# Kernel optimization log

Measured on AMD Instinct MI355X. Metric: run time of the kernel, lower is better.

Reference implementation:

```python
import jax, jax.numpy as jnp
import numpy as np

STEPS = 32
LO, HI = 0.0, 1.0
BETA = 0.1
IMPULSE = float(1.0 / (abs(BETA) * np.sqrt(np.pi)))  # unused in fwd, kept for parity


def _cells(x):
    """Filtration values of all cells of the V-construction cubical complex.
    Vertices = pixels; edges = max of the 2 endpoint pixels; squares = max of 4 corners."""
    v = x                                                    # [B,C,H,W]   sign +1
    he = jnp.maximum(x[..., :, :-1], x[..., :, 1:])          # [B,C,H,W-1] sign -1
    ve = jnp.maximum(x[..., :-1, :], x[..., 1:, :])          # [B,C,H-1,W] sign -1
    sq = jnp.maximum(jnp.maximum(x[..., :-1, :-1], x[..., :-1, 1:]),
                     jnp.maximum(x[..., 1:, :-1], x[..., 1:, 1:]))  # [B,C,H-1,W-1] sign +1
    return v, he, ve, sq


def _ecc_forward(x):
    """Euler characteristic curve ECC(t) = #V(t) - #E(t) + #F(t) sampled on
    tseq = linspace(LO, HI, STEPS). Returns [B, C*STEPS] (flattened, matching nn.Flatten)."""
    B, C, H, W = x.shape
    BC = B * C
    tseq = jnp.linspace(LO, HI, STEPS, dtype=x.dtype)
    v, he, ve, sq = _cells(x)
    f = jnp.concatenate([v.reshape(BC, -1), he.reshape(BC, -1),
                         ve.reshape(BC, -1), sq.reshape(BC, -1)], axis=1)  # [BC, Ncells]
    signs = jnp.concatenate([
        jnp.ones(H * W, jnp.float32),
        -jnp.ones(H * (W - 1), jnp.float32),
        -jnp.ones((H - 1) * W, jnp.float32),
        jnp.ones((H - 1) * (W - 1), jnp.float32),
    ])
    # first threshold index j with tseq[j] >= f (cell is "alive" for all t >= idx)
    idx = jnp.searchsorted(tseq, f, side='left')            # [BC, Ncells], values in [0, STEPS]
    rows = jnp.arange(BC)[:, None]
    hist = jnp.zeros((BC, STEPS + 1), jnp.float32).at[rows, idx].add(signs[None, :])
    ecc = jnp.cumsum(hist[:, :STEPS], axis=1)               # [BC, STEPS]
    return ecc.reshape(B, C * STEPS)


def setup_inputs() -> dict:
    key = jax.random.key(0)
    x = jax.random.uniform(key, (64, 3, 224, 224), dtype=jnp.float32)
    return {"x": x}


def reference(x):
    return _ecc_forward(x)
```

## Files before the change

### kernel.cpp

```cpp
#include <hip/hip_runtime.h>
#include <hip/hip_bf16.h>


#define H 224
#define W 224
#define STEPS 32
#define NBINS 33
#define NCOL 64
#define BANDS 8
#define BAND_ROWS 28
#define SUB_ROWS 7
#define NTHR 256

__device__ __forceinline__ int bin_of(float f) {
    return (int)fmaf(f, 31.0f, 0.99999994f);
}

struct BinState {
    int B0, B1, B2, B3, Bn, Bp;
};

__device__ __forceinline__ void pair1_update(int* __restrict__ lhc,
                                             const BinState& S)
{
    int dm = (S.B0 > S.Bp) ? 1 : 0;
    int d0 = (S.B1 > S.B0) ? 1 : 0;
    int d1 = (S.B2 > S.B1) ? 1 : 0;
    int d2 = (S.B3 > S.B2) ? 1 : 0;
    int d3 = (S.Bn > S.B3) ? 1 : 0;
    atomicAdd(&lhc[S.B0 << 6], d0 - dm);
    atomicAdd(&lhc[S.B1 << 6], d1 - d0);
    atomicAdd(&lhc[S.B2 << 6], d2 - d1);
    atomicAdd(&lhc[S.B3 << 6], d3 - d2);
}

__device__ __forceinline__ void pair2_update_roll(int* __restrict__ lhc,
                                                  BinState& S, float4 G,
                                                  bool lastc, bool firstc)
{
    int C0 = bin_of(G.x), C1 = bin_of(G.y), C2 = bin_of(G.z), C3 = bin_of(G.w);
    int t;
    t = __shfl_down(C0, 1); int Cn = lastc  ? 64 : t;
    t = __shfl_up  (C3, 1); int Cp = firstc ? 63 : t;

    int M0 = max(S.B0, C0), M1 = max(S.B1, C1),
        M2 = max(S.B2, C2), M3 = max(S.B3, C3);
    int Mn = max(S.Bn, Cn), Mp = max(S.Bp, Cp);
    int em = (M0 > Mp) ? 1 : 0;
    int e0 = (M1 > M0) ? 1 : 0;
    int e1 = (M2 > M1) ? 1 : 0;
    int e2 = (M3 > M2) ? 1 : 0;
    int e3 = (Mn > M3) ? 1 : 0;
    atomicAdd(&lhc[M0 << 6], em - e0);
    atomicAdd(&lhc[M1 << 6], e0 - e1);
    atomicAdd(&lhc[M2 << 6], e1 - e2);
    atomicAdd(&lhc[M3 << 6], e2 - e3);

    S.B0 = C0; S.B1 = C1; S.B2 = C2; S.B3 = C3; S.Bn = Cn; S.Bp = Cp;
}

__global__ __launch_bounds__(NTHR, 6) void ecc_fused_kernel(
        const float* __restrict__ x, float* __restrict__ out)
{
    __shared__ int lh[NBINS * NCOL];
    __shared__ int bins[STEPS];

    const int tid = threadIdx.x;
    for (int i = tid; i < NBINS * NCOL; i += NTHR) lh[i] = 0;
    __syncthreads();

    const int band = blockIdx.x & (BANDS - 1);
    const int img  = blockIdx.x / BANDS;
    const float* __restrict__ p = x + (size_t)img * (H * W);

    const int c = tid & 63;
    const int s = tid >> 6;

    if (c < 56) {
        const bool lastc  = (c == 55);
        const bool firstc = (c == 0);
        const int  r0 = band * BAND_ROWS + s * SUB_ROWS;
        int* __restrict__ lhc = lh + c;

        const float* __restrict__ row = p + r0 * W + (c << 2);
        float4 F = *(const float4*)row;
        BinState S;
        S.B0 = bin_of(F.x); S.B1 = bin_of(F.y);
        S.B2 = bin_of(F.z); S.B3 = bin_of(F.w);
        int t;
        t = __shfl_down(S.B0, 1); S.Bn = lastc  ? 64 : t;
        t = __shfl_up  (S.B3, 1); S.Bp = firstc ? 63 : t;

        if (r0 != H - SUB_ROWS) {
            #pragma unroll
            for (int k = 0; k < SUB_ROWS; ++k) {
                pair1_update(lhc, S);
                float4 G = *(const float4*)(row + W);
                pair2_update_roll(lhc, S, G, lastc, firstc);
                row += W;
            }
        } else {
            #pragma unroll
            for (int k = 0; k < SUB_ROWS - 1; ++k) {
                pair1_update(lhc, S);
                float4 G = *(const float4*)(row + W);
                pair2_update_roll(lhc, S, G, lastc, firstc);
                row += W;
            }
            pair1_update(lhc, S);
        }
    }
    __syncthreads();

    const int b = tid >> 3;
    const int g = tid & 7;
    const int4* rowp = (const int4*)(lh + (b << 6) + (g << 3));
    int4 u0 = rowp[0], u1 = rowp[1];
    int sum = u0.x + u0.y + u0.z + u0.w + u1.x + u1.y + u1.z + u1.w;
    sum += __shfl_xor(sum, 1);
    sum += __shfl_xor(sum, 2);
    sum += __shfl_xor(sum, 4);
    if (g == 0) bins[b] = sum;
    __syncthreads();

    if (tid < STEPS) {
        int v = bins[tid];
        #pragma unroll
        for (int off = 1; off < STEPS; off <<= 1) {
            int u = __shfl_up(v, off);
            if (tid >= off) v += u;
        }
        atomicAdd(&out[img * STEPS + tid], (float)v);
    }
}

extern "C" void kernel_launch(void* const* d_in, const int* in_sizes, int n_in,
                              void* d_out, int out_size, void* d_ws, size_t ws_size,
                              hipStream_t stream) {
    const float* x = (const float*)d_in[0];
    float* out = (float*)d_out;

    const int nimg = in_sizes[0] / (H * W);

    dim3 grid(nimg * BANDS);
    ecc_fused_kernel<<<grid, NTHR, 0, stream>>>(x, out);
}
```

Baseline: 75.44 us.

## Replace LDS atomics with private per-thread packed 16-bit histogram slabs

Each thread now owns a private column in a per-subrow slab, so histogram updates become plain read-modify-write instead of LDS atomicAdd. Two bins are packed per 32-bit word as biased 16-bit counters, which halves the number of words per slab. The final reduction unpacks and sums the four slabs and subtracts the bias. The cost is extra shift and mask work in the reduction and a reliance on the bias keeping each packed counter from underflowing or carrying into its neighbour.

```diff
diff --git a/kernel.cpp b/kernel.cpp
--- a/kernel.cpp
+++ b/kernel.cpp
@@ -1,26 +1,31 @@
 #include <hip/hip_runtime.h>
-#include <hip/hip_bf16.h>
 
 
 #define H 224
 #define W 224
 #define STEPS 32
-#define NBINS 33
+#define NWORDS 17
 #define NCOL 64
+#define SLAB (NWORDS * NCOL)
 #define BANDS 8
 #define BAND_ROWS 28
 #define SUB_ROWS 7
 #define NTHR 256
+#define BIASW 0x00400040
 
 __device__ __forceinline__ int bin_of(float f) {
     return (int)fmaf(f, 31.0f, 0.99999994f);
+}
+
+__device__ __forceinline__ void hist_add(int* __restrict__ lhw, int bin, int v) {
+    lhw[(bin >> 1) << 6] += (v << ((bin & 1) << 4));
 }
 
 struct BinState {
     int B0, B1, B2, B3, Bn, Bp;
 };
 
-__device__ __forceinline__ void pair1_update(int* __restrict__ lhc,
+__device__ __forceinline__ void pair1_update(int* __restrict__ lhw,
                                              const BinState& S)
 {
     int dm = (S.B0 > S.Bp) ? 1 : 0;
@@ -28,13 +33,13 @@
     int d1 = (S.B2 > S.B1) ? 1 : 0;
     int d2 = (S.B3 > S.B2) ? 1 : 0;
     int d3 = (S.Bn > S.B3) ? 1 : 0;
-    atomicAdd(&lhc[S.B0 << 6], d0 - dm);
-    atomicAdd(&lhc[S.B1 << 6], d1 - d0);
-    atomicAdd(&lhc[S.B2 << 6], d2 - d1);
-    atomicAdd(&lhc[S.B3 << 6], d3 - d2);
+    hist_add(lhw, S.B0, d0 - dm);
+    hist_add(lhw, S.B1, d1 - d0);
+    hist_add(lhw, S.B2, d2 - d1);
+    hist_add(lhw, S.B3, d3 - d2);
 }
 
-__device__ __forceinline__ void pair2_update_roll(int* __restrict__ lhc,
+__device__ __forceinline__ void pair2_update_roll(int* __restrict__ lhw,
                                                   BinState& S, float4 G,
                                                   bool lastc, bool firstc)
 {
@@ -51,10 +56,10 @@
     int e1 = (M2 > M1) ? 1 : 0;
     int e2 = (M3 > M2) ? 1 : 0;
     int e3 = (Mn > M3) ? 1 : 0;
-    atomicAdd(&lhc[M0 << 6], em - e0);
-    atomicAdd(&lhc[M1 << 6], e0 - e1);
-    atomicAdd(&lhc[M2 << 6], e1 - e2);
-    atomicAdd(&lhc[M3 << 6], e2 - e3);
+    hist_add(lhw, M0, em - e0);
+    hist_add(lhw, M1, e0 - e1);
+    hist_add(lhw, M2, e1 - e2);
+    hist_add(lhw, M3, e2 - e3);
 
     S.B0 = C0; S.B1 = C1; S.B2 = C2; S.B3 = C3; S.Bn = Cn; S.Bp = Cp;
 }
@@ -62,11 +67,11 @@
 __global__ __launch_bounds__(NTHR, 6) void ecc_fused_kernel(
         const float* __restrict__ x, float* __restrict__ out)
 {
-    __shared__ int lh[NBINS * NCOL];
+    __shared__ int lh[4 * SLAB];
     __shared__ int bins[STEPS];
 
     const int tid = threadIdx.x;
-    for (int i = tid; i < NBINS * NCOL; i += NTHR) lh[i] = 0;
+    for (int i = tid; i < 4 * SLAB; i += NTHR) lh[i] = BIASW;
     __syncthreads();
 
     const int band = blockIdx.x & (BANDS - 1);
@@ -80,7 +85,7 @@
         const bool lastc  = (c == 55);
         const bool firstc = (c == 0);
         const int  r0 = band * BAND_ROWS + s * SUB_ROWS;
-        int* __restrict__ lhc = lh + c;
+        int* __restrict__ lhw = lh + s * SLAB + c;
 
         const float* __restrict__ row = p + r0 * W + (c << 2);
         float4 F = *(const float4*)row;
@@ -94,33 +99,41 @@
         if (r0 != H - SUB_ROWS) {
             #pragma unroll
             for (int k = 0; k < SUB_ROWS; ++k) {
-                pair1_update(lhc, S);
+                pair1_update(lhw, S);
                 float4 G = *(const float4*)(row + W);
-                pair2_update_roll(lhc, S, G, lastc, firstc);
+                pair2_update_roll(lhw, S, G, lastc, firstc);
                 row += W;
             }
         } else {
             #pragma unroll
             for (int k = 0; k < SUB_ROWS - 1; ++k) {
-                pair1_update(lhc, S);
+                pair1_update(lhw, S);
                 float4 G = *(const float4*)(row + W);
-                pair2_update_roll(lhc, S, G, lastc, firstc);
+                pair2_update_roll(lhw, S, G, lastc, firstc);
                 row += W;
             }
-            pair1_update(lhc, S);
+            pair1_update(lhw, S);
         }
     }
     __syncthreads();
 
     const int b = tid >> 3;
     const int g = tid & 7;
-    const int4* rowp = (const int4*)(lh + (b << 6) + (g << 3));
-    int4 u0 = rowp[0], u1 = rowp[1];
-    int sum = u0.x + u0.y + u0.z + u0.w + u1.x + u1.y + u1.z + u1.w;
+    const int hsh = (b & 1) << 4;
+    int sum = 0;
+    #pragma unroll
+    for (int s2 = 0; s2 < 4; ++s2) {
+        const int4* rp = (const int4*)(lh + s2 * SLAB + ((b >> 1) << 6) + (g << 3));
+        int4 u0 = rp[0], u1 = rp[1];
+        sum += ((u0.x >> hsh) & 0xFFFF) + ((u0.y >> hsh) & 0xFFFF)
+             + ((u0.z >> hsh) & 0xFFFF) + ((u0.w >> hsh) & 0xFFFF)
+             + ((u1.x >> hsh) & 0xFFFF) + ((u1.y >> hsh) & 0xFFFF)
+             + ((u1.z >> hsh) & 0xFFFF) + ((u1.w >> hsh) & 0xFFFF);
+    }
     sum += __shfl_xor(sum, 1);
     sum += __shfl_xor(sum, 2);
     sum += __shfl_xor(sum, 4);
-    if (g == 0) bins[b] = sum;
+    if (g == 0) bins[b] = sum - 64 * 256;
     __syncthreads();
 
     if (tid < STEPS) {
```

Result: no change. 76.89 us (+1.9%).

## Stage all rows via async global-to-LDS loads with staged vmcnt waits

Applied to the files above, without the earlier changes.

Issues all eight row loads per wave up front as direct global-to-LDS transfers, then waits on a decreasing vmcnt so each row's histogram work can start as soon as that row arrives. This puts all of a wave's memory requests in flight at once instead of one load per iteration. It adds about 28KB of LDS per block and lowers the launch-bounds occupancy hint from 6 to 4. The last band duplicates row 6 into slot 7 so the load count stays uniform. Correctness depends on the in-order vmcnt semantics of LDS-direct loads and on each wave reading only its own staging slice without a barrier.

```diff
diff --git a/kernel.cpp b/kernel.cpp
--- a/kernel.cpp
+++ b/kernel.cpp
@@ -1,5 +1,4 @@
 #include <hip/hip_runtime.h>
-#include <hip/hip_bf16.h>
 
 
 #define H 224
@@ -12,6 +11,12 @@
 #define SUB_ROWS 7
 #define NTHR 256
 
+#define VMWAIT(N) do { asm volatile("s_waitcnt vmcnt(" #N ")" ::: "memory"); \
+                       __builtin_amdgcn_sched_barrier(0); } while (0)
+
+typedef __attribute__((address_space(3))) void       lds_void_t;
+typedef const __attribute__((address_space(1))) void glb_void_t;
+
 __device__ __forceinline__ int bin_of(float f) {
     return (int)fmaf(f, 31.0f, 0.99999994f);
 }
@@ -19,6 +24,16 @@
 struct BinState {
     int B0, B1, B2, B3, Bn, Bp;
 };
+
+__device__ __forceinline__ void init_state(BinState& S, float4 F,
+                                           bool lastc, bool firstc)
+{
+    S.B0 = bin_of(F.x); S.B1 = bin_of(F.y);
+    S.B2 = bin_of(F.z); S.B3 = bin_of(F.w);
+    int t;
+    t = __shfl_down(S.B0, 1); S.Bn = lastc  ? 64 : t;
+    t = __shfl_up  (S.B3, 1); S.Bp = firstc ? 63 : t;
+}
 
 __device__ __forceinline__ void pair1_update(int* __restrict__ lhc,
                                              const BinState& S)
@@ -59,13 +74,15 @@
     S.B0 = C0; S.B1 = C1; S.B2 = C2; S.B3 = C3; S.Bn = Cn; S.Bp = Cp;
 }
 
-__global__ __launch_bounds__(NTHR, 6) void ecc_fused_kernel(
+__global__ __launch_bounds__(NTHR, 4) void ecc_fused_kernel(
         const float* __restrict__ x, float* __restrict__ out)
 {
+    __shared__ float stage[4][8][W];
     __shared__ int lh[NBINS * NCOL];
     __shared__ int bins[STEPS];
 
-    const int tid = threadIdx.x;
+    const int tid  = threadIdx.x;
+
     for (int i = tid; i < NBINS * NCOL; i += NTHR) lh[i] = 0;
     __syncthreads();
 
@@ -75,39 +92,72 @@
 
     const int c = tid & 63;
     const int s = tid >> 6;
+    const int r0 = band * BAND_ROWS + s * SUB_ROWS;
 
     if (c < 56) {
-        const bool lastc  = (c == 55);
-        const bool firstc = (c == 0);
-        const int  r0 = band * BAND_ROWS + s * SUB_ROWS;
+        const bool lastc    = (c == 55);
+        const bool firstc   = (c == 0);
+        const bool interior = (r0 != H - SUB_ROWS);
         int* __restrict__ lhc = lh + c;
 
-        const float* __restrict__ row = p + r0 * W + (c << 2);
-        float4 F = *(const float4*)row;
+        const float* __restrict__ base = p + (size_t)r0 * W + (c << 2);
+        {
+            #pragma unroll
+            for (int r = 0; r < 7; ++r) {
+                __builtin_amdgcn_global_load_lds(
+                    (glb_void_t*)(base + r * W),
+                    (lds_void_t*)&stage[s][r][0], 16, 0, 0);
+            }
+            const int r7 = interior ? 7 : 6;
+            __builtin_amdgcn_global_load_lds(
+                (glb_void_t*)(base + r7 * W),
+                (lds_void_t*)&stage[s][7][0], 16, 0, 0);
+        }
+
         BinState S;
-        S.B0 = bin_of(F.x); S.B1 = bin_of(F.y);
-        S.B2 = bin_of(F.z); S.B3 = bin_of(F.w);
-        int t;
-        t = __shfl_down(S.B0, 1); S.Bn = lastc  ? 64 : t;
-        t = __shfl_up  (S.B3, 1); S.Bp = firstc ? 63 : t;
-
-        if (r0 != H - SUB_ROWS) {
-            #pragma unroll
-            for (int k = 0; k < SUB_ROWS; ++k) {
-                pair1_update(lhc, S);
-                float4 G = *(const float4*)(row + W);
-                pair2_update_roll(lhc, S, G, lastc, firstc);
-                row += W;
-            }
-        } else {
-            #pragma unroll
-            for (int k = 0; k < SUB_ROWS - 1; ++k) {
-                pair1_update(lhc, S);
-                float4 G = *(const float4*)(row + W);
-                pair2_update_roll(lhc, S, G, lastc, firstc);
-                row += W;
-            }
+        VMWAIT(6);
+        float4 F0 = *(const float4*)&stage[s][0][c << 2];
+        init_state(S, F0, lastc, firstc);
+        pair1_update(lhc, S);
+        {
+            float4 G = *(const float4*)&stage[s][1][c << 2];
+            pair2_update_roll(lhc, S, G, lastc, firstc);
             pair1_update(lhc, S);
+        }
+        VMWAIT(5);
+        {
+            float4 G = *(const float4*)&stage[s][2][c << 2];
+            pair2_update_roll(lhc, S, G, lastc, firstc);
+            pair1_update(lhc, S);
+        }
+        VMWAIT(4);
+        {
+            float4 G = *(const float4*)&stage[s][3][c << 2];
+            pair2_update_roll(lhc, S, G, lastc, firstc);
+            pair1_update(lhc, S);
+        }
+        VMWAIT(3);
+        {
+            float4 G = *(const float4*)&stage[s][4][c << 2];
+            pair2_update_roll(lhc, S, G, lastc, firstc);
+            pair1_update(lhc, S);
+        }
+        VMWAIT(2);
+        {
+            float4 G = *(const float4*)&stage[s][5][c << 2];
+            pair2_update_roll(lhc, S, G, lastc, firstc);
+            pair1_update(lhc, S);
+        }
+        VMWAIT(1);
+        {
+            float4 G = *(const float4*)&stage[s][6][c << 2];
+            pair2_update_roll(lhc, S, G, lastc, firstc);
+            pair1_update(lhc, S);
+        }
+        if (interior) {
+            VMWAIT(0);
+            float4 G = *(const float4*)&stage[s][7][c << 2];
+            pair2_update_roll(lhc, S, G, lastc, firstc);
         }
     }
     __syncthreads();
```

Measured after the change: 77.12 us. +2.2%, slower.
